# Optimization experiments

Measured on AMD Instinct MI355X. Metric: run time of the kernel, lower is better.

The kernel has to match this reference:

```python
import jax, jax.numpy as jnp
import numpy as np

DIM = 2048
N_HEADS = 16
HEAD_DIM = DIM // N_HEADS  # 128
B, T = 8, 1024


def setup_inputs() -> dict:
    key = jax.random.key(0)
    ks = jax.random.split(key, 5)
    s_in = 1.0 / np.sqrt(DIM)
    return {
        "x": jax.random.normal(ks[0], (B, T, DIM), dtype=jnp.float32),
        "W_qkv": jax.random.uniform(ks[1], (DIM + 2 * HEAD_DIM, DIM), dtype=jnp.float32, minval=-s_in, maxval=s_in),
        "b_qkv": jax.random.uniform(ks[2], (DIM + 2 * HEAD_DIM,), dtype=jnp.float32, minval=-s_in, maxval=s_in),
        "W_out": jax.random.uniform(ks[3], (DIM, DIM), dtype=jnp.float32, minval=-s_in, maxval=s_in),
        "b_out": jax.random.uniform(ks[4], (DIM,), dtype=jnp.float32, minval=-s_in, maxval=s_in),
    }


def reference(x, W_qkv, b_qkv, W_out, b_out):
    Bx, Tx, D = x.shape
    H, hd = N_HEADS, HEAD_DIM
    qkv = x @ W_qkv.T + b_qkv                      # [B,T,D+2*hd]
    q = qkv[:, :, :D].reshape(Bx, Tx, H, hd).transpose(0, 2, 1, 3)  # [B,H,T,hd]
    k = qkv[:, :, D:D + hd]                        # [B,T,hd] (shared head)
    v = qkv[:, :, D + hd:]                         # [B,T,hd]
    # torch repeat(1,1,H).view(B,T,H,hd) duplicates the single KV head -> broadcast instead
    scores = jnp.einsum('bhtd,bsd->bhts', q, k) / jnp.sqrt(jnp.asarray(hd, x.dtype))
    causal = jnp.tril(jnp.ones((Tx, Tx), dtype=bool))
    scores = jnp.where(causal[None, None], scores, jnp.asarray(-jnp.inf, x.dtype))
    att = jax.nn.softmax(scores, axis=-1)          # [B,H,T,T]
    out = jnp.einsum('bhts,bsd->bhtd', att, v)     # [B,H,T,hd]
    out = out.transpose(0, 2, 1, 3).reshape(Bx, Tx, D)
    return out @ W_out.T + b_out
```

## Files before the change

### kernel.cpp

```cpp
#include <hip/hip_runtime.h>
#include <hip/hip_bf16.h>
#include <math.h>
#include <stdint.h>

#define DIM 2048
#define NH 16
#define HD 128
#define BB 8
#define TT 1024
#define NROW (BB*TT)
#define QKVD (DIM + 2*HD)

typedef unsigned short u16;
typedef unsigned int u32;
typedef float f32x4 __attribute__((ext_vector_type(4)));
typedef u32 u32x4 __attribute__((ext_vector_type(4)));
typedef __bf16 bf16x8 __attribute__((ext_vector_type(8)));

__device__ inline u16 f2bf(float f) {
  u32 u = __builtin_bit_cast(u32, f);
  u += 0x7FFF + ((u >> 16) & 1);
  return (u16)(u >> 16);
}

__device__ inline u32 cvt_pk_bf16(float lo, float hi) {
  u32 d;
  asm("v_cvt_pk_bf16_f32 %0, %1, %2" : "=v"(d) : "v"(lo), "v"(hi));
  return d;
}

__device__ inline void gload_lds16(const void* g, void* l) {
  __builtin_amdgcn_global_load_lds(
      (const __attribute__((address_space(1))) void*)g,
      (__attribute__((address_space(3))) void*)l,
      16, 0, 0);
}

__global__ void cvt_f32_bf16(const float* __restrict__ in, u16* __restrict__ out, int n4) {
  int i = blockIdx.x * blockDim.x + threadIdx.x;
  int st = gridDim.x * blockDim.x;
  for (; i < n4; i += st) {
    float4 v = reinterpret_cast<const float4*>(in)[i];
    ushort4 o;
    o.x = f2bf(v.x); o.y = f2bf(v.y); o.z = f2bf(v.z); o.w = f2bf(v.w);
    reinterpret_cast<ushort4*>(out)[i] = o;
  }
}

template<bool OUT_BF16, bool WRITE_VT>
__global__ __launch_bounds__(256, 2) void gemm_nt(
    const u16* __restrict__ A, const u16* __restrict__ Bm,
    const float* __restrict__ bias, void* __restrict__ Cout,
    u16* __restrict__ vT, int K, int Mcols)
{
  __shared__ u16 As[128*32];
  __shared__ u16 Bs[128*32];
  const int tid = threadIdx.x;
  const int w = tid >> 6, l = tid & 63;
  const int wm = w >> 1, wn = w & 1;
  const int rl = l & 15, gl = l >> 4;
  const int rowBase = blockIdx.x * 128;
  const int colBase = blockIdx.y * 128;

  f32x4 acc[4][4] = {};

  for (int k0 = 0; k0 < K; k0 += 32) {
    __syncthreads();
#pragma unroll
    for (int i = 0; i < 2; ++i) {
      int c = i*256 + w*64 + l;
      int r = c >> 2, kc = c & 3;
      gload_lds16(A  + (size_t)(rowBase + r)*K + k0 + kc*8, &As[(i*256 + w*64)*8]);
      gload_lds16(Bm + (size_t)(colBase + r)*K + k0 + kc*8, &Bs[(i*256 + w*64)*8]);
    }
    __syncthreads();

    bf16x8 af[4], bf[4];
#pragma unroll
    for (int fm = 0; fm < 4; ++fm)
      af[fm] = *(const bf16x8*)&As[(wm*64 + fm*16 + rl)*32 + gl*8];
#pragma unroll
    for (int fn = 0; fn < 4; ++fn)
      bf[fn] = *(const bf16x8*)&Bs[(wn*64 + fn*16 + rl)*32 + gl*8];
#pragma unroll
    for (int fm = 0; fm < 4; ++fm)
#pragma unroll
      for (int fn = 0; fn < 4; ++fn)
        acc[fm][fn] = __builtin_amdgcn_mfma_f32_16x16x32_bf16(af[fm], bf[fn], acc[fm][fn], 0, 0, 0);
  }

  float bv[4];
#pragma unroll
  for (int fn = 0; fn < 4; ++fn) bv[fn] = bias[colBase + wn*64 + fn*16 + rl];

#pragma unroll
  for (int fm = 0; fm < 4; ++fm) {
#pragma unroll
    for (int fn = 0; fn < 4; ++fn) {
      const int col = colBase + wn*64 + fn*16 + rl;
#pragma unroll
      for (int r = 0; r < 4; ++r) {
        const int row = rowBase + wm*64 + fm*16 + gl*4 + r;
        float v = acc[fm][fn][r] + bv[fn];
        if (OUT_BF16) ((u16*)Cout)[(size_t)row*Mcols + col] = f2bf(v);
        else          ((float*)Cout)[(size_t)row*Mcols + col] = v;
        if (WRITE_VT) {
          if (col >= DIM + HD) {
            int d = col - (DIM + HD);
            int b = row >> 10, t = row & 1023;
            vT[((size_t)(b*HD + d) << 10) + t] = f2bf(v);
          }
        }
      }
    }
  }
}

__global__ __launch_bounds__(256, 2) void mqa_attn(
    const u16* __restrict__ qkv, const u16* __restrict__ vT,
    u16* __restrict__ attout)
{
  __shared__ char lds[65536];

  const int tid = threadIdx.x;
  const int wid = tid >> 6, l = tid & 63;
  const int rl = l & 15, gl = l >> 4;
  const int qi = blockIdx.x;
  const int b = blockIdx.y >> 4, h = blockIdx.y & 15;
  const int qrow0 = qi*64 + wid*16;
  const float scale = 0.08838834764831845f;

  const u16* kbase = qkv + (size_t)b*TT*QKVD + DIM;
  const u16* vbase = vT + ((size_t)b*HD << 10);

  auto STAGE = [&](int buf, int s0) {
    char* kl = lds + buf*32768;
    char* vl = kl + 16384;
#pragma unroll
    for (int i = 0; i < 4; ++i) {
      int L = wid*4096 + i*1024 + l*16;
      int s = L >> 8, kb = (L & 255) ^ ((s & 7) << 4);
      gload_lds16(kbase + (size_t)(s0 + s)*QKVD + (kb >> 1), kl + wid*4096 + i*1024);
      int d = L >> 7, sb = (L & 127) ^ ((d & 7) << 4);
      gload_lds16(vbase + ((size_t)d << 10) + s0 + (sb >> 1), vl + wid*4096 + i*1024);
    }
  };

  STAGE(0, 0);
  asm volatile("" ::: "memory");

  bf16x8 qf[4];
  {
    const u16* qp = qkv + (size_t)(b*TT + qrow0 + rl)*QKVD + h*HD + gl*8;
#pragma unroll
    for (int kk = 0; kk < 4; ++kk) qf[kk] = *(const bf16x8*)(qp + kk*32);
  }

  f32x4 accO[8] = {};
  float mrow = -INFINITY, lrow = 0.f;
  const int tg = qrow0 + rl;
  const int addrA = (((gl & 1) * 2) * 16 + rl) * 4;
  const int addrB = addrA + 64;
  const bool hiSel = (gl >= 2);

  for (int it = 0; it <= qi; ++it) {
    if (it < qi) {
      STAGE((it + 1) & 1, (it + 1) << 6);
      asm volatile("s_waitcnt vmcnt(8)" ::: "memory");
    } else {
      asm volatile("s_waitcnt vmcnt(0)" ::: "memory");
    }
    __builtin_amdgcn_s_barrier();

    const char* kl = lds + (it & 1)*32768;
    const char* vl = kl + 16384;
    const int s0 = it << 6;

    f32x4 sc[4] = {};
    __builtin_amdgcn_s_setprio(1);
#pragma unroll
    for (int fs = 0; fs < 4; ++fs) {
      const int s = fs*16 + rl;
#pragma unroll
      for (int kkd = 0; kkd < 4; ++kkd) {
        bf16x8 kf = *(const bf16x8*)(kl + ((s*256 + kkd*64 + gl*16) ^ ((s & 7) << 4)));
        sc[fs] = __builtin_amdgcn_mfma_f32_16x16x32_bf16(kf, qf[kkd], sc[fs], 0, 0, 0);
      }
    }
    __builtin_amdgcn_s_setprio(0);

    float mx = -INFINITY;
#pragma unroll
    for (int fs = 0; fs < 4; ++fs)
#pragma unroll
      for (int r = 0; r < 4; ++r) {
        int sg = s0 + fs*16 + gl*4 + r;
        float v = sc[fs][r] * scale;
        v = (sg > tg) ? -INFINITY : v;
        sc[fs][r] = v;
        mx = fmaxf(mx, v);
      }
    mx = fmaxf(mx, __shfl_xor(mx, 16));
    mx = fmaxf(mx, __shfl_xor(mx, 32));
    float mnew = fmaxf(mrow, mx);
    float rr = __expf(mrow - mnew);
    float ps = 0.f;
#pragma unroll
    for (int fs = 0; fs < 4; ++fs)
#pragma unroll
      for (int r = 0; r < 4; ++r) {
        float p = __expf(sc[fs][r] - mnew);
        sc[fs][r] = p;
        ps += p;
      }
    ps += __shfl_xor(ps, 16);
    ps += __shfl_xor(ps, 32);
    mrow = mnew;
    lrow = lrow * rr + ps;
#pragma unroll
    for (int fd = 0; fd < 8; ++fd)
#pragma unroll
      for (int r = 0; r < 4; ++r) accO[fd][r] *= rr;

    u32 pw[4][2];
#pragma unroll
    for (int fs = 0; fs < 4; ++fs) {
      pw[fs][0] = cvt_pk_bf16(sc[fs][0], sc[fs][1]);
      pw[fs][1] = cvt_pk_bf16(sc[fs][2], sc[fs][3]);
    }
    u32x4 bw[2];
#pragma unroll
    for (int kk = 0; kk < 2; ++kk)
#pragma unroll
      for (int w = 0; w < 4; ++w) {
        int addr = (w < 2) ? addrA : addrB;
        u32 lo = __builtin_amdgcn_ds_bpermute(addr, (int)pw[2*kk + 0][w & 1]);
        u32 hi = __builtin_amdgcn_ds_bpermute(addr, (int)pw[2*kk + 1][w & 1]);
        bw[kk][w] = hiSel ? hi : lo;
      }

    __builtin_amdgcn_s_setprio(1);
#pragma unroll
    for (int kk = 0; kk < 2; ++kk) {
      bf16x8 pb = __builtin_bit_cast(bf16x8, bw[kk]);
#pragma unroll
      for (int fd = 0; fd < 8; ++fd) {
        const int d = fd*16 + rl;
        bf16x8 vf = *(const bf16x8*)(vl + ((d*128 + kk*64 + gl*16) ^ ((d & 7) << 4)));
        accO[fd] = __builtin_amdgcn_mfma_f32_16x16x32_bf16(vf, pb, accO[fd], 0, 0, 0);
      }
    }
    __builtin_amdgcn_s_setprio(0);

    __builtin_amdgcn_s_barrier();
  }

  const float inv = 1.0f / lrow;
  u16* outp = attout + (size_t)(b*TT + tg)*DIM + h*HD;
#pragma unroll
  for (int fd = 0; fd < 8; ++fd) {
    ushort4 o;
    o.x = f2bf(accO[fd][0] * inv);
    o.y = f2bf(accO[fd][1] * inv);
    o.z = f2bf(accO[fd][2] * inv);
    o.w = f2bf(accO[fd][3] * inv);
    *(ushort4*)(outp + fd*16 + gl*4) = o;
  }
}

extern "C" void kernel_launch(void* const* d_in, const int* in_sizes, int n_in,
                              void* d_out, int out_size, void* d_ws, size_t ws_size,
                              hipStream_t stream) {
  const float* x    = (const float*)d_in[0];
  const float* Wqkv = (const float*)d_in[1];
  const float* bqkv = (const float*)d_in[2];
  const float* Wout = (const float*)d_in[3];
  const float* bout = (const float*)d_in[4];

  char* ws = (char*)d_ws;
  u16* xb    = (u16*)(ws);
  u16* wqb   = (u16*)(ws + 33554432);
  u16* qkvb  = (u16*)(ws + 33554432 + 9437184);
  u16* vtb   = (u16*)(ws + 33554432 + 9437184 + 37748736);
  u16* attb  = xb;
  u16* woutb = wqb;

  cvt_f32_bf16<<<2048, 256, 0, stream>>>(x,    xb,  NROW*DIM/4);
  cvt_f32_bf16<<<2048, 256, 0, stream>>>(Wqkv, wqb, QKVD*DIM/4);

  dim3 g1(NROW/128, QKVD/128);
  gemm_nt<true, true><<<g1, 256, 0, stream>>>(xb, wqb, bqkv, qkvb, vtb, DIM, QKVD);

  cvt_f32_bf16<<<2048, 256, 0, stream>>>(Wout, woutb, DIM*DIM/4);

  dim3 ga(TT/64, BB*NH);
  mqa_attn<<<ga, 256, 0, stream>>>(qkvb, vtb, attb);

  dim3 g2(NROW/128, DIM/128);
  gemm_nt<false, false><<<g2, 256, 0, stream>>>(attb, woutb, bout, d_out, nullptr, DIM, DIM);
}
```

Measured before the change: 352.9 us.

## Use 128-row query blocks with 8 waves, fold scale into Q, lazy softmax rescale

The attention kernel now uses 512-thread blocks covering 128 query rows, so each staged K/V tile is shared by twice as many waves. Blocks are launched in reverse order so the long causal rows start first. The softmax scale times log2(e) is folded into Q in the QKV GEMM epilogue, letting the loop use exp2 directly and apply the causal mask only on the diagonal tile. The running-max rescale of the output accumulator is skipped while the new max stays within 8 of the old one. Waves whose rows lie above a tile idle through barriers, and a launch bound of 4 blocks of 512 threads tightens the register budget, which could cause spills.

```diff
diff --git a/kernel.cpp b/kernel.cpp
--- a/kernel.cpp
+++ b/kernel.cpp
@@ -16,6 +16,8 @@
 typedef float f32x4 __attribute__((ext_vector_type(4)));
 typedef u32 u32x4 __attribute__((ext_vector_type(4)));
 typedef __bf16 bf16x8 __attribute__((ext_vector_type(8)));
+
+#define QSCALE_LOG2E (0.08838834764831845f * 1.4426950408889634f)
 
 __device__ inline u16 f2bf(float f) {
   u32 u = __builtin_bit_cast(u32, f);
@@ -102,21 +104,20 @@
       for (int r = 0; r < 4; ++r) {
         const int row = rowBase + wm*64 + fm*16 + gl*4 + r;
         float v = acc[fm][fn][r] + bv[fn];
-        if (OUT_BF16) ((u16*)Cout)[(size_t)row*Mcols + col] = f2bf(v);
-        else          ((float*)Cout)[(size_t)row*Mcols + col] = v;
-        if (WRITE_VT) {
-          if (col >= DIM + HD) {
-            int d = col - (DIM + HD);
-            int b = row >> 10, t = row & 1023;
-            vT[((size_t)(b*HD + d) << 10) + t] = f2bf(v);
-          }
-        }
-      }
-    }
-  }
-}
-
-__global__ __launch_bounds__(256, 2) void mqa_attn(
+        if (WRITE_VT && col >= DIM + HD) {
+          int d = col - (DIM + HD);
+          int b = row >> 10, t = row & 1023;
+          vT[((size_t)(b*HD + d) << 10) + t] = f2bf(v);
+        }
+        float vs = (WRITE_VT && col < DIM) ? v * QSCALE_LOG2E : v;
+        if (OUT_BF16) ((u16*)Cout)[(size_t)row*Mcols + col] = f2bf(vs);
+        else          ((float*)Cout)[(size_t)row*Mcols + col] = vs;
+      }
+    }
+  }
+}
+
+__global__ __launch_bounds__(512, 4) void mqa_attn(
     const u16* __restrict__ qkv, const u16* __restrict__ vT,
     u16* __restrict__ attout)
 {
@@ -125,10 +126,11 @@
   const int tid = threadIdx.x;
   const int wid = tid >> 6, l = tid & 63;
   const int rl = l & 15, gl = l >> 4;
-  const int qi = blockIdx.x;
+  const int qb = (int)gridDim.x - 1 - (int)blockIdx.x;
   const int b = blockIdx.y >> 4, h = blockIdx.y & 15;
-  const int qrow0 = qi*64 + wid*16;
-  const float scale = 0.08838834764831845f;
+  const int qrow0 = qb*128 + wid*16;
+  const int diag = qrow0 >> 6;
+  const int itmax = 2*qb + 1;
 
   const u16* kbase = qkv + (size_t)b*TT*QKVD + DIM;
   const u16* vbase = vT + ((size_t)b*HD << 10);
@@ -137,12 +139,12 @@
     char* kl = lds + buf*32768;
     char* vl = kl + 16384;
 #pragma unroll
-    for (int i = 0; i < 4; ++i) {
-      int L = wid*4096 + i*1024 + l*16;
+    for (int i = 0; i < 2; ++i) {
+      int L = (i*8 + wid)*1024 + l*16;
       int s = L >> 8, kb = (L & 255) ^ ((s & 7) << 4);
-      gload_lds16(kbase + (size_t)(s0 + s)*QKVD + (kb >> 1), kl + wid*4096 + i*1024);
+      gload_lds16(kbase + (size_t)(s0 + s)*QKVD + (kb >> 1), kl + (i*8 + wid)*1024);
       int d = L >> 7, sb = (L & 127) ^ ((d & 7) << 4);
-      gload_lds16(vbase + ((size_t)d << 10) + s0 + (sb >> 1), vl + wid*4096 + i*1024);
+      gload_lds16(vbase + ((size_t)d << 10) + s0 + (sb >> 1), vl + (i*8 + wid)*1024);
     }
   };
 
@@ -163,94 +165,104 @@
   const int addrB = addrA + 64;
   const bool hiSel = (gl >= 2);
 
-  for (int it = 0; it <= qi; ++it) {
-    if (it < qi) {
+  for (int it = 0; it <= itmax; ++it) {
+    if (it < itmax) {
       STAGE((it + 1) & 1, (it + 1) << 6);
-      asm volatile("s_waitcnt vmcnt(8)" ::: "memory");
+      asm volatile("s_waitcnt vmcnt(4)" ::: "memory");
     } else {
       asm volatile("s_waitcnt vmcnt(0)" ::: "memory");
     }
     __builtin_amdgcn_s_barrier();
 
-    const char* kl = lds + (it & 1)*32768;
-    const char* vl = kl + 16384;
-    const int s0 = it << 6;
-
-    f32x4 sc[4] = {};
-    __builtin_amdgcn_s_setprio(1);
-#pragma unroll
-    for (int fs = 0; fs < 4; ++fs) {
-      const int s = fs*16 + rl;
-#pragma unroll
-      for (int kkd = 0; kkd < 4; ++kkd) {
-        bf16x8 kf = *(const bf16x8*)(kl + ((s*256 + kkd*64 + gl*16) ^ ((s & 7) << 4)));
-        sc[fs] = __builtin_amdgcn_mfma_f32_16x16x32_bf16(kf, qf[kkd], sc[fs], 0, 0, 0);
-      }
-    }
-    __builtin_amdgcn_s_setprio(0);
-
-    float mx = -INFINITY;
-#pragma unroll
-    for (int fs = 0; fs < 4; ++fs)
-#pragma unroll
-      for (int r = 0; r < 4; ++r) {
-        int sg = s0 + fs*16 + gl*4 + r;
-        float v = sc[fs][r] * scale;
-        v = (sg > tg) ? -INFINITY : v;
-        sc[fs][r] = v;
-        mx = fmaxf(mx, v);
-      }
-    mx = fmaxf(mx, __shfl_xor(mx, 16));
-    mx = fmaxf(mx, __shfl_xor(mx, 32));
-    float mnew = fmaxf(mrow, mx);
-    float rr = __expf(mrow - mnew);
-    float ps = 0.f;
-#pragma unroll
-    for (int fs = 0; fs < 4; ++fs)
-#pragma unroll
-      for (int r = 0; r < 4; ++r) {
-        float p = __expf(sc[fs][r] - mnew);
-        sc[fs][r] = p;
-        ps += p;
-      }
-    ps += __shfl_xor(ps, 16);
-    ps += __shfl_xor(ps, 32);
-    mrow = mnew;
-    lrow = lrow * rr + ps;
-#pragma unroll
-    for (int fd = 0; fd < 8; ++fd)
-#pragma unroll
-      for (int r = 0; r < 4; ++r) accO[fd][r] *= rr;
-
-    u32 pw[4][2];
-#pragma unroll
-    for (int fs = 0; fs < 4; ++fs) {
-      pw[fs][0] = cvt_pk_bf16(sc[fs][0], sc[fs][1]);
-      pw[fs][1] = cvt_pk_bf16(sc[fs][2], sc[fs][3]);
-    }
-    u32x4 bw[2];
-#pragma unroll
-    for (int kk = 0; kk < 2; ++kk)
-#pragma unroll
-      for (int w = 0; w < 4; ++w) {
-        int addr = (w < 2) ? addrA : addrB;
-        u32 lo = __builtin_amdgcn_ds_bpermute(addr, (int)pw[2*kk + 0][w & 1]);
-        u32 hi = __builtin_amdgcn_ds_bpermute(addr, (int)pw[2*kk + 1][w & 1]);
-        bw[kk][w] = hiSel ? hi : lo;
-      }
-
-    __builtin_amdgcn_s_setprio(1);
-#pragma unroll
-    for (int kk = 0; kk < 2; ++kk) {
-      bf16x8 pb = __builtin_bit_cast(bf16x8, bw[kk]);
-#pragma unroll
-      for (int fd = 0; fd < 8; ++fd) {
-        const int d = fd*16 + rl;
-        bf16x8 vf = *(const bf16x8*)(vl + ((d*128 + kk*64 + gl*16) ^ ((d & 7) << 4)));
-        accO[fd] = __builtin_amdgcn_mfma_f32_16x16x32_bf16(vf, pb, accO[fd], 0, 0, 0);
-      }
-    }
-    __builtin_amdgcn_s_setprio(0);
+    if (it <= diag) {
+      const char* kl = lds + (it & 1)*32768;
+      const char* vl = kl + 16384;
+
+      f32x4 sc[4] = {};
+      __builtin_amdgcn_s_setprio(1);
+#pragma unroll
+      for (int fs = 0; fs < 4; ++fs) {
+        const int s = fs*16 + rl;
+#pragma unroll
+        for (int kkd = 0; kkd < 4; ++kkd) {
+          bf16x8 kf = *(const bf16x8*)(kl + ((s*256 + kkd*64 + gl*16) ^ ((s & 7) << 4)));
+          sc[fs] = __builtin_amdgcn_mfma_f32_16x16x32_bf16(kf, qf[kkd], sc[fs], 0, 0, 0);
+        }
+      }
+      __builtin_amdgcn_s_setprio(0);
+
+      if (it == diag) {
+        const int s0 = it << 6;
+#pragma unroll
+        for (int fs = 0; fs < 4; ++fs)
+#pragma unroll
+          for (int r = 0; r < 4; ++r) {
+            int sg = s0 + fs*16 + gl*4 + r;
+            if (sg > tg) sc[fs][r] = -INFINITY;
+          }
+      }
+
+      float mx = -INFINITY;
+#pragma unroll
+      for (int fs = 0; fs < 4; ++fs)
+        mx = fmaxf(mx, fmaxf(fmaxf(sc[fs][0], sc[fs][1]), fmaxf(sc[fs][2], sc[fs][3])));
+      mx = fmaxf(mx, __shfl_xor(mx, 16));
+      mx = fmaxf(mx, __shfl_xor(mx, 32));
+
+      if (!__all(mx <= mrow + 8.f)) {
+        float mnew = fmaxf(mrow, mx);
+        float rr = __builtin_amdgcn_exp2f(mrow - mnew);
+#pragma unroll
+        for (int fd = 0; fd < 8; ++fd)
+#pragma unroll
+          for (int r = 0; r < 4; ++r) accO[fd][r] *= rr;
+        lrow *= rr;
+        mrow = mnew;
+      }
+
+      float ps = 0.f;
+#pragma unroll
+      for (int fs = 0; fs < 4; ++fs)
+#pragma unroll
+        for (int r = 0; r < 4; ++r) {
+          float p = __builtin_amdgcn_exp2f(sc[fs][r] - mrow);
+          sc[fs][r] = p;
+          ps += p;
+        }
+      ps += __shfl_xor(ps, 16);
+      ps += __shfl_xor(ps, 32);
+      lrow += ps;
+
+      u32 pw[4][2];
+#pragma unroll
+      for (int fs = 0; fs < 4; ++fs) {
+        pw[fs][0] = cvt_pk_bf16(sc[fs][0], sc[fs][1]);
+        pw[fs][1] = cvt_pk_bf16(sc[fs][2], sc[fs][3]);
+      }
+      u32x4 bw[2];
+#pragma unroll
+      for (int kk = 0; kk < 2; ++kk)
+#pragma unroll
+        for (int w = 0; w < 4; ++w) {
+          int addr = (w < 2) ? addrA : addrB;
+          u32 lo = __builtin_amdgcn_ds_bpermute(addr, (int)pw[2*kk + 0][w & 1]);
+          u32 hi = __builtin_amdgcn_ds_bpermute(addr, (int)pw[2*kk + 1][w & 1]);
+          bw[kk][w] = hiSel ? hi : lo;
+        }
+
+      __builtin_amdgcn_s_setprio(1);
+#pragma unroll
+      for (int kk = 0; kk < 2; ++kk) {
+        bf16x8 pb = __builtin_bit_cast(bf16x8, bw[kk]);
+#pragma unroll
+        for (int fd = 0; fd < 8; ++fd) {
+          const int d = fd*16 + rl;
+          bf16x8 vf = *(const bf16x8*)(vl + ((d*128 + kk*64 + gl*16) ^ ((d & 7) << 4)));
+          accO[fd] = __builtin_amdgcn_mfma_f32_16x16x32_bf16(vf, pb, accO[fd], 0, 0, 0);
+        }
+      }
+      __builtin_amdgcn_s_setprio(0);
+    }
 
     __builtin_amdgcn_s_barrier();
   }
@@ -293,8 +305,8 @@
 
   cvt_f32_bf16<<<2048, 256, 0, stream>>>(Wout, woutb, DIM*DIM/4);
 
-  dim3 ga(TT/64, BB*NH);
-  mqa_attn<<<ga, 256, 0, stream>>>(qkvb, vtb, attb);
+  dim3 ga(TT/128, BB*NH);
+  mqa_attn<<<ga, 512, 0, stream>>>(qkvb, vtb, attb);
 
   dim3 g2(NROW/128, DIM/128);
   gemm_nt<false, false><<<g2, 256, 0, stream>>>(attb, woutb, bout, d_out, nullptr, DIM, DIM);
```

New measurement: 325.5 us. 7.8% less time.
